# Performance work log

Measured on AMD Instinct MI355X. Metric: run time of the kernel, lower is better.

The kernel has to match this reference:

```python
import jax, jax.numpy as jnp
import numpy as np

B, L, D_IN = 32, 1024, 256
EMB, OUT = 128, 128


def setup_inputs() -> dict:
    key = jax.random.key(0)
    ks = jax.random.split(key, 8)
    traj = jax.random.normal(ks[0], (B, L, D_IN), dtype=jnp.float32)
    traj_length = jax.random.randint(ks[1], (B,), 0, L).astype(jnp.int64)
    s_in = 1.0 / np.sqrt(D_IN)
    W_ge = jax.random.uniform(ks[2], (D_IN, EMB), jnp.float32, -s_in, s_in)
    b_ge = jax.random.uniform(ks[3], (EMB,), jnp.float32, -s_in, s_in)
    W_eg = jax.random.uniform(ks[4], (D_IN, EMB), jnp.float32, -s_in, s_in)
    b_eg = jax.random.uniform(ks[5], (EMB,), jnp.float32, -s_in, s_in)
    Wg = jax.random.normal(ks[6], (EMB, OUT), dtype=jnp.float32)
    ln_gamma = jnp.ones((OUT,), jnp.float32)
    ln_beta = jnp.zeros((OUT,), jnp.float32)
    return {"traj": traj, "traj_length": traj_length, "W_ge": W_ge, "b_ge": b_ge,
            "W_eg": W_eg, "b_eg": b_eg, "Wg": Wg, "ln_gamma": ln_gamma, "ln_beta": ln_beta}


def layer_norm(x, gamma, beta, eps=1e-5):
    mu = jnp.mean(x, axis=-1, keepdims=True)
    var = jnp.var(x, axis=-1, keepdims=True)
    return (x - mu) * jax.lax.rsqrt(var + eps) * gamma + beta


def reference(traj, traj_length, W_ge, b_ge, W_eg, b_eg, Wg, ln_gamma, ln_beta):
    Bd, Ld, _ = traj.shape
    # node embeddings for similarity
    EA = traj @ W_ge + b_ge                                   # [B, L, EMB]
    sim = jax.nn.relu(jnp.einsum('bie,bje->bij', EA, EA))     # [B, L, L]
    mask = (jnp.arange(Ld)[None, :] < traj_length[:, None]).astype(jnp.float32)  # [B, L]
    # NOTE: original zeroes masked scores (not -inf); exp(0)=1 still contributes
    sim = sim * mask[:, None, :]
    A = jax.nn.softmax(sim, axis=-1)                          # [B, L, L]
    Eg = traj @ W_eg + b_eg                                   # [B, L, EMB]
    theta = Eg @ Wg                                           # [B, L, OUT]
    propagated = jnp.einsum('bij,bjd->bid', A, theta)         # [B, L, OUT]
    propagated = layer_norm(propagated, ln_gamma, ln_beta)
    return propagated * mask[:, :, None]
```

## Files before the change

kernel.cpp:

```cpp
#include <hip/hip_runtime.h>
#include <hip/hip_bf16.h>

#define B_   32
#define L_   1024
#define DIN  256

typedef __bf16 bf16x8 __attribute__((ext_vector_type(8)));
typedef float  f32x4  __attribute__((ext_vector_type(4)));
typedef unsigned short u16;

union U8 { u16 s[8]; bf16x8 v; };
union VU { uint2 p[2]; bf16x8 v; };

__device__ __forceinline__ u16 f2b(float f) {
  union { float f; unsigned u; } v; v.f = f;
  unsigned r = (v.u + 0x7FFFu + ((v.u >> 16) & 1u)) >> 16;
  return (u16)r;
}
__device__ __forceinline__ float b2f(u16 h) {
  union { unsigned u; float f; } c; c.u = ((unsigned)h) << 16;
  return c.f;
}

#define TR16_0(dst, addr) \
  asm volatile("ds_read_b64_tr_b16 %0, %1 offset:0" : "=&v"(dst) : "v"(addr))
#define TR16_128(dst, addr) \
  asm volatile("ds_read_b64_tr_b16 %0, %1 offset:128" : "=&v"(dst) : "v"(addr))

__global__ __launch_bounds__(256) void k_fold(
    const float* __restrict__ W_ge, const float* __restrict__ b_eg,
    const float* __restrict__ W_eg, const float* __restrict__ Wg,
    u16* __restrict__ WbT, float* __restrict__ bc, float* __restrict__ TT) {
  int idx = blockIdx.x * 256 + threadIdx.x;
  if (idx < 32768) {
    int d = idx >> 7, o = idx & 127;
    float s = 0.f;
    for (int k = 0; k < 128; ++k) s += W_eg[d * 128 + k] * Wg[k * 128 + o];
    WbT[(128 + o) * 256 + d] = f2b(s);
  } else if (idx < 65536) {
    int i = idx - 32768; int d = i >> 7, o = i & 127;
    WbT[o * 256 + d] = f2b(W_ge[d * 128 + o]);
  } else if (idx < 65664) {
    int o = idx - 65536;
    float s = 0.f;
    for (int k = 0; k < 128; ++k) s += b_eg[k] * Wg[k * 128 + o];
    bc[o] = s;
  } else if (idx < 65664 + 4096) {
    TT[idx - 65664] = 0.f;
  }
}

__global__ __launch_bounds__(512) void k_embed(
    const float* __restrict__ traj, const u16* __restrict__ WbT,
    const float* __restrict__ b_ge, const float* __restrict__ bc,
    const int* __restrict__ lens,
    u16* __restrict__ EA, u16* __restrict__ TH, float* __restrict__ TT) {
  __shared__ u16 Ws[256][264];
  __shared__ float tailLds[128];
  const int tid = threadIdx.x;
  const int wv = tid >> 6, ln = tid & 63;
  const int li = ln & 15, g = ln >> 4;
  const int b   = blockIdx.x >> 3;
  const int rl0 = (blockIdx.x & 7) * 128;
  const int len = lens[b];
  const int rw  = rl0 + wv * 16 + li;
  const size_t row = (size_t)b * L_ + rw;
  const int nd0 = (rl0 >= len) ? 8 : 0;
  const bool doTail = (rl0 + 128 > len);

  if (tid < 128) tailLds[tid] = 0.f;

  {
    const u16* src = &WbT[(tid >> 1) * 256 + (tid & 1) * 128];
    u16* dst = &Ws[tid >> 1][(tid & 1) * 128];
#pragma unroll
    for (int i = 0; i < 16; ++i)
      *(bf16x8*)&dst[i * 8] = *(const bf16x8*)&src[i * 8];
  }

  bf16x8 tf[8];
  {
    const float* tp = &traj[row * DIN];
#pragma unroll
    for (int t = 0; t < 8; ++t) {
      float4 v0 = *(const float4*)(tp + t * 32 + g * 8);
      float4 v1 = *(const float4*)(tp + t * 32 + g * 8 + 4);
      U8 bu;
      bu.s[0]=f2b(v0.x); bu.s[1]=f2b(v0.y); bu.s[2]=f2b(v0.z); bu.s[3]=f2b(v0.w);
      bu.s[4]=f2b(v1.x); bu.s[5]=f2b(v1.y); bu.s[6]=f2b(v1.z); bu.s[7]=f2b(v1.w);
      tf[t] = bu.v;
    }
  }
  __syncthreads();

  f32x4 acc[16] = {};
#pragma unroll
  for (int kc = 0; kc < 8; ++kc) {
#pragma unroll
    for (int nd = 0; nd < 16; ++nd) {
      if (nd >= nd0) {
        bf16x8 afrag = *(const bf16x8*)&Ws[nd * 16 + li][kc * 32 + g * 8];
        acc[nd] = __builtin_amdgcn_mfma_f32_16x16x32_bf16(afrag, tf[kc], acc[nd], 0, 0, 0);
      }
    }
  }

#pragma unroll
  for (int nd = 0; nd < 16; ++nd) {
    if (nd < nd0) continue;
    int ncol = nd * 16 + 4 * g;
    float fv[4];
    u16 pk[4];
#pragma unroll
    for (int r = 0; r < 4; ++r) {
      int n = ncol + r;
      float bias = (n < 128) ? b_ge[n] : bc[n - 128];
      fv[r] = acc[nd][r] + bias;
      pk[r] = f2b(fv[r]);
    }
    u16* dst = (ncol < 128) ? &EA[row * 128 + ncol]
                            : &TH[row * 128 + (ncol - 128)];
    *(uint2*)dst = *(uint2*)pk;

    if (nd >= 8 && doTail) {
      float tv[4];
#pragma unroll
      for (int r = 0; r < 4; ++r) tv[r] = (rw >= len) ? fv[r] : 0.f;
#pragma unroll
      for (int d = 1; d < 16; d <<= 1)
#pragma unroll
        for (int r = 0; r < 4; ++r) tv[r] += __shfl_xor(tv[r], d, 16);
      if (li == 0) {
#pragma unroll
        for (int r = 0; r < 4; ++r)
          atomicAdd(&tailLds[(nd - 8) * 16 + 4 * g + r], tv[r]);
      }
    }
  }
  __syncthreads();
  if (tid < 128) {
    float v = tailLds[tid];
    if (v != 0.f) atomicAdd(&TT[b * 128 + tid], v);
  }
}

#define PSTR 40

__global__ __launch_bounds__(256) void k_attn(
    const u16* __restrict__ EA, const u16* __restrict__ TH,
    const float* __restrict__ TT, const int* __restrict__ lens,
    const float* __restrict__ gamma, const float* __restrict__ beta,
    float* __restrict__ out) {
  const int b  = blockIdx.y;
  const int i0 = blockIdx.x * 32;
  const int len = lens[b];
  const int tid = threadIdx.x;
  const size_t obase = ((size_t)b * L_ + i0) * 128;

  if (i0 >= len) {
    float4 z = {0.f, 0.f, 0.f, 0.f};
    for (int q = tid; q < 1024; q += 256) *(float4*)&out[obase + (size_t)q * 4] = z;
    return;
  }

  __shared__ u16 Kl[2][2][4096];
  __shared__ u16 Vl[2][2][4096];
  __shared__ u16 Pl[4][640];
  __shared__ float MLm[32], MLl[32];
  __shared__ u16 MGb[32][136];

  const int wv = tid >> 6;
  const int h = wv & 1, p = wv >> 1;
  const int ln = tid & 63, li = ln & 15, g = ln >> 4;
  const int ptid = tid & 127;
  const int jr = ptid >> 2, ch = ptid & 3;
  const size_t ebase = (size_t)b * L_ * 128;

  u16* pl = Pl[wv];

  bf16x8 qf[4];
  {
    const u16* qp = &EA[ebase + (size_t)(i0 + h * 16 + li) * 128 + g * 8];
#pragma unroll
    for (int kc = 0; kc < 4; ++kc) qf[kc] = *(const bf16x8*)&qp[kc * 32];
  }

  f32x4 Oa[8] = {};
  float m[4] = {0.f, 0.f, 0.f, 0.f};
  float lsum[4] = {0.f, 0.f, 0.f, 0.f};

  const int njt = (len + 31) >> 5;
  const int kiter = (njt + 1) >> 1;

  bf16x8 kreg[4], vreg[4];
  {
    const int t0 = (p < njt) ? p : (njt - 1);
    const u16* ks = &EA[ebase + (size_t)(t0 * 32 + jr) * 128];
    const u16* vs = &TH[ebase + (size_t)(t0 * 32 + jr) * 128];
#pragma unroll
    for (int k = 0; k < 4; ++k) {
      kreg[k] = *(const bf16x8*)(ks + (ch + 4 * k) * 8);
      vreg[k] = *(const bf16x8*)(vs + (ch + 4 * k) * 8);
    }
  }

  for (int kk = 0; kk < kiter; ++kk) {
    const int t = 2 * kk + p;
    u16* kd = Kl[p][kk & 1];
    u16* vd = Vl[p][kk & 1];
#pragma unroll
    for (int k = 0; k < 4; ++k) {
      int cq = ch + 4 * k;
      int cb = cq * 16;
      *(bf16x8*)((char*)kd + jr * 256 + (cb ^ ((jr & 7) << 4))) = kreg[k];
      *(bf16x8*)&vd[(cq >> 1) * 512 + jr * 16 + (cq & 1) * 8] = vreg[k];
    }
    if (kk + 1 < kiter) {
      int tn = 2 * (kk + 1) + p; if (tn > njt - 1) tn = njt - 1;
      const u16* ks = &EA[ebase + (size_t)(tn * 32 + jr) * 128];
      const u16* vs = &TH[ebase + (size_t)(tn * 32 + jr) * 128];
#pragma unroll
      for (int k = 0; k < 4; ++k) {
        kreg[k] = *(const bf16x8*)(ks + (ch + 4 * k) * 8);
        vreg[k] = *(const bf16x8*)(vs + (ch + 4 * k) * 8);
      }
    }
    __syncthreads();
    if (t < njt) {
      const int j0 = t * 32;
      f32x4 S[2] = {};
#pragma unroll
      for (int n = 0; n < 2; ++n) {
        int krow = n * 16 + li;
        const char* kb = (const char*)kd + krow * 256;
#pragma unroll
        for (int kc = 0; kc < 4; ++kc) {
          bf16x8 kf = *(const bf16x8*)(kb + ((kc * 64 + g * 16) ^ ((krow & 7) << 4)));
          S[n] = __builtin_amdgcn_mfma_f32_16x16x32_bf16(qf[kc], kf, S[n], 0, 0, 0);
        }
      }
      const unsigned vtr = (unsigned)(size_t)vd + g * 256 + li * 8;
      uint2 vr[16];
#pragma unroll
      for (int t8 = 0; t8 < 8; ++t8) {
        unsigned a = vtr + t8 * 1024;
        TR16_0(vr[2 * t8], a);
        TR16_128(vr[2 * t8 + 1], a);
      }
      const bool v0 = (j0 + li) < len;
      const bool v1 = (j0 + 16 + li) < len;
      float x[4];
#pragma unroll
      for (int r = 0; r < 4; ++r) {
        float s0 = v0 ? fmaxf(S[0][r], 0.f) : 0.f;
        float s1 = v1 ? fmaxf(S[1][r], 0.f) : 0.f;
        S[0][r] = s0; S[1][r] = s1;
        x[r] = fmaxf(s0, s1);
      }
#pragma unroll
      for (int d = 1; d < 16; d <<= 1)
#pragma unroll
        for (int r = 0; r < 4; ++r) x[r] = fmaxf(x[r], __shfl_xor(x[r], d, 16));

      float p0[4], p1[4], fac[4], y[4];
#pragma unroll
      for (int r = 0; r < 4; ++r) {
        float mt = fmaxf(m[r], x[r]);
        fac[r] = __expf(m[r] - mt);
        m[r] = mt;
        p0[r] = v0 ? __expf(S[0][r] - mt) : 0.f;
        p1[r] = v1 ? __expf(S[1][r] - mt) : 0.f;
        y[r] = p0[r] + p1[r];
      }
#pragma unroll
      for (int d = 1; d < 16; d <<= 1)
#pragma unroll
        for (int r = 0; r < 4; ++r) y[r] += __shfl_xor(y[r], d, 16);
#pragma unroll
      for (int r = 0; r < 4; ++r) lsum[r] = lsum[r] * fac[r] + y[r];
#pragma unroll
      for (int t8 = 0; t8 < 8; ++t8)
#pragma unroll
        for (int r = 0; r < 4; ++r) Oa[t8][r] *= fac[r];

#pragma unroll
      for (int r = 0; r < 4; ++r) {
        pl[(4 * g + r) * PSTR + li]      = f2b(p0[r]);
        pl[(4 * g + r) * PSTR + 16 + li] = f2b(p1[r]);
      }
      bf16x8 pf = *(const bf16x8*)&pl[li * PSTR + g * 8];

      asm volatile("s_waitcnt lgkmcnt(0)" ::: "memory");
      __builtin_amdgcn_sched_barrier(0);

#pragma unroll
      for (int t8 = 0; t8 < 8; ++t8) {
        VU vu; vu.p[0] = vr[2 * t8]; vu.p[1] = vr[2 * t8 + 1];
        Oa[t8] = __builtin_amdgcn_mfma_f32_16x16x32_bf16(pf, vu.v, Oa[t8], 0, 0, 0);
      }
    }
  }

  __syncthreads();
  if (p == 1) {
#pragma unroll
    for (int r = 0; r < 4; ++r) {
      int rr = h * 16 + 4 * g + r;
      if (li == 0) { MLm[rr] = m[r]; MLl[rr] = lsum[r]; }
#pragma unroll
      for (int t8 = 0; t8 < 8; ++t8)
        MGb[rr][t8 * 16 + li] = f2b(Oa[t8][r]);
    }
  }
  __syncthreads();
  if (p != 0) return;

#pragma unroll
  for (int r = 0; r < 4; ++r) {
    int rr = h * 16 + 4 * g + r;
    float m1 = MLm[rr], l1 = MLl[rr];
    float ms = fmaxf(m[r], m1);
    float f0 = __expf(m[r] - ms), f1 = __expf(m1 - ms);
    lsum[r] = lsum[r] * f0 + l1 * f1;
    m[r] = ms;
#pragma unroll
    for (int t8 = 0; t8 < 8; ++t8)
      Oa[t8][r] = Oa[t8][r] * f0 + b2f(MGb[rr][t8 * 16 + li]) * f1;
  }

  {
    float tt8[8];
#pragma unroll
    for (int t8 = 0; t8 < 8; ++t8) tt8[t8] = TT[b * 128 + t8 * 16 + li];
#pragma unroll
    for (int r = 0; r < 4; ++r) {
      float wt = __expf(-m[r]);
      lsum[r] += wt * (float)(L_ - len);
#pragma unroll
      for (int t8 = 0; t8 < 8; ++t8) Oa[t8][r] += wt * tt8[t8];
    }
  }

  float sm[4] = {0.f, 0.f, 0.f, 0.f}, sq[4] = {0.f, 0.f, 0.f, 0.f};
#pragma unroll
  for (int r = 0; r < 4; ++r) {
    float inv = 1.f / lsum[r];
#pragma unroll
    for (int t8 = 0; t8 < 8; ++t8) {
      float val = Oa[t8][r] * inv;
      Oa[t8][r] = val;
      sm[r] += val; sq[r] += val * val;
    }
  }
#pragma unroll
  for (int d = 1; d < 16; d <<= 1)
#pragma unroll
    for (int r = 0; r < 4; ++r) {
      sm[r] += __shfl_xor(sm[r], d, 16);
      sq[r] += __shfl_xor(sq[r], d, 16);
    }

  const int irow = i0 + h * 16;
#pragma unroll
  for (int r = 0; r < 4; ++r) {
    float mu   = sm[r] * (1.f / 128.f);
    float var  = sq[r] * (1.f / 128.f) - mu * mu;
    float rstd = rsqrtf(var + 1e-5f);
    int i = irow + 4 * g + r;
    bool valid = i < len;
#pragma unroll
    for (int t8 = 0; t8 < 8; ++t8) {
      int dcol = t8 * 16 + li;
      float o = valid ? ((Oa[t8][r] - mu) * rstd * gamma[dcol] + beta[dcol]) : 0.f;
      out[((size_t)b * L_ + i) * 128 + dcol] = o;
    }
  }
}

extern "C" void kernel_launch(void* const* d_in, const int* in_sizes, int n_in,
                              void* d_out, int out_size, void* d_ws, size_t ws_size,
                              hipStream_t stream) {
  const float* traj  = (const float*)d_in[0];
  const int*   lens  = (const int*)d_in[1];
  const float* W_ge  = (const float*)d_in[2];
  const float* b_ge  = (const float*)d_in[3];
  const float* W_eg  = (const float*)d_in[4];
  const float* b_eg  = (const float*)d_in[5];
  const float* Wg    = (const float*)d_in[6];
  const float* gamma = (const float*)d_in[7];
  const float* beta  = (const float*)d_in[8];
  float* out = (float*)d_out;

  char* ws = (char*)d_ws;
  u16*   WbT = (u16*)ws;
  float* bc  = (float*)(ws + 131072);
  float* TT  = (float*)(ws + 131072 + 512);
  u16*   EA  = (u16*)(ws + 131072 + 512 + 16384);
  u16*   TH  = EA + (size_t)B_ * L_ * 128;

  k_fold<<<273, 256, 0, stream>>>(W_ge, b_eg, W_eg, Wg, WbT, bc, TT);
  k_embed<<<256, 512, 0, stream>>>(traj, WbT, b_ge, bc, lens, EA, TH, TT);
  k_attn<<<dim3(32, 32), 256, 0, stream>>>(EA, TH, TT, lens, gamma, beta, out);
}
```

Baseline: 173.7 us.

## Stage Wg in LDS for weight folding and stream embed weights from global

k_fold now has each block copy Wg into a 64 KB shared buffer. Each thread then computes one folded W_eg·Wg entry from LDS instead of re-reading Wg from global memory, and the blocks are remapped so each one covers two input rows. k_embed drops the 132 KB LDS copy of the packed weights and its per-block setup. It uses 64-row blocks of 256 threads, doubling the block count, and reads MFMA weight fragments straight from global memory through the cache. traj is now loaded and converted to bf16 inside the k loop rather than all up front. This trades LDS staging and occupancy limits for more global/L2 traffic on weight reads.

```diff
diff --git a/kernel.cpp b/kernel.cpp
--- a/kernel.cpp
+++ b/kernel.cpp
@@ -31,76 +31,71 @@
     const float* __restrict__ W_ge, const float* __restrict__ b_eg,
     const float* __restrict__ W_eg, const float* __restrict__ Wg,
     u16* __restrict__ WbT, float* __restrict__ bc, float* __restrict__ TT) {
-  int idx = blockIdx.x * 256 + threadIdx.x;
-  if (idx < 32768) {
-    int d = idx >> 7, o = idx & 127;
+  __shared__ float WgL[128 * 128];
+  const int blk = blockIdx.x, tid = threadIdx.x;
+  if (blk < 128) {
+    const float4* src = (const float4*)Wg;
+    float4* dst = (float4*)WgL;
+#pragma unroll
+    for (int i = 0; i < 16; ++i) dst[tid + i * 256] = src[tid + i * 256];
+    __syncthreads();
+    const int d = blk * 2 + (tid >> 7);
+    const int o = tid & 127;
+    const float* we = &W_eg[d * 128];
     float s = 0.f;
-    for (int k = 0; k < 128; ++k) s += W_eg[d * 128 + k] * Wg[k * 128 + o];
+#pragma unroll 8
+    for (int k = 0; k < 128; ++k) s += we[k] * WgL[k * 128 + o];
     WbT[(128 + o) * 256 + d] = f2b(s);
-  } else if (idx < 65536) {
-    int i = idx - 32768; int d = i >> 7, o = i & 127;
+  } else if (blk < 256) {
+    int i = (blk - 128) * 256 + tid;
+    int d = i >> 7, o = i & 127;
     WbT[o * 256 + d] = f2b(W_ge[d * 128 + o]);
-  } else if (idx < 65664) {
-    int o = idx - 65536;
-    float s = 0.f;
-    for (int k = 0; k < 128; ++k) s += b_eg[k] * Wg[k * 128 + o];
-    bc[o] = s;
-  } else if (idx < 65664 + 4096) {
-    TT[idx - 65664] = 0.f;
-  }
-}
-
-__global__ __launch_bounds__(512) void k_embed(
+  } else {
+    int i = (blk - 256) * 256 + tid;
+    if (i < 128) {
+      float s = 0.f;
+      for (int k = 0; k < 128; ++k) s += b_eg[k] * Wg[k * 128 + i];
+      bc[i] = s;
+    } else if (i < 128 + 4096) {
+      TT[i - 128] = 0.f;
+    }
+  }
+}
+
+__global__ __launch_bounds__(256) void k_embed(
     const float* __restrict__ traj, const u16* __restrict__ WbT,
     const float* __restrict__ b_ge, const float* __restrict__ bc,
     const int* __restrict__ lens,
     u16* __restrict__ EA, u16* __restrict__ TH, float* __restrict__ TT) {
-  __shared__ u16 Ws[256][264];
   __shared__ float tailLds[128];
   const int tid = threadIdx.x;
   const int wv = tid >> 6, ln = tid & 63;
   const int li = ln & 15, g = ln >> 4;
-  const int b   = blockIdx.x >> 3;
-  const int rl0 = (blockIdx.x & 7) * 128;
+  const int b   = blockIdx.x >> 4;
+  const int rl0 = (blockIdx.x & 15) * 64;
   const int len = lens[b];
   const int rw  = rl0 + wv * 16 + li;
   const size_t row = (size_t)b * L_ + rw;
   const int nd0 = (rl0 >= len) ? 8 : 0;
-  const bool doTail = (rl0 + 128 > len);
+  const bool doTail = (rl0 + 64 > len);
 
   if (tid < 128) tailLds[tid] = 0.f;
-
-  {
-    const u16* src = &WbT[(tid >> 1) * 256 + (tid & 1) * 128];
-    u16* dst = &Ws[tid >> 1][(tid & 1) * 128];
-#pragma unroll
-    for (int i = 0; i < 16; ++i)
-      *(bf16x8*)&dst[i * 8] = *(const bf16x8*)&src[i * 8];
-  }
-
-  bf16x8 tf[8];
-  {
-    const float* tp = &traj[row * DIN];
-#pragma unroll
-    for (int t = 0; t < 8; ++t) {
-      float4 v0 = *(const float4*)(tp + t * 32 + g * 8);
-      float4 v1 = *(const float4*)(tp + t * 32 + g * 8 + 4);
-      U8 bu;
-      bu.s[0]=f2b(v0.x); bu.s[1]=f2b(v0.y); bu.s[2]=f2b(v0.z); bu.s[3]=f2b(v0.w);
-      bu.s[4]=f2b(v1.x); bu.s[5]=f2b(v1.y); bu.s[6]=f2b(v1.z); bu.s[7]=f2b(v1.w);
-      tf[t] = bu.v;
-    }
-  }
   __syncthreads();
 
   f32x4 acc[16] = {};
-#pragma unroll
+  const float* tp = &traj[row * DIN];
+
   for (int kc = 0; kc < 8; ++kc) {
+    float4 v0 = *(const float4*)(tp + kc * 32 + g * 8);
+    float4 v1 = *(const float4*)(tp + kc * 32 + g * 8 + 4);
+    U8 bu;
+    bu.s[0]=f2b(v0.x); bu.s[1]=f2b(v0.y); bu.s[2]=f2b(v0.z); bu.s[3]=f2b(v0.w);
+    bu.s[4]=f2b(v1.x); bu.s[5]=f2b(v1.y); bu.s[6]=f2b(v1.z); bu.s[7]=f2b(v1.w);
 #pragma unroll
     for (int nd = 0; nd < 16; ++nd) {
       if (nd >= nd0) {
-        bf16x8 afrag = *(const bf16x8*)&Ws[nd * 16 + li][kc * 32 + g * 8];
-        acc[nd] = __builtin_amdgcn_mfma_f32_16x16x32_bf16(afrag, tf[kc], acc[nd], 0, 0, 0);
+        bf16x8 afrag = *(const bf16x8*)&WbT[(nd * 16 + li) * 256 + kc * 32 + g * 8];
+        acc[nd] = __builtin_amdgcn_mfma_f32_16x16x32_bf16(afrag, bu.v, acc[nd], 0, 0, 0);
       }
     }
   }
@@ -399,6 +394,6 @@
   u16*   TH  = EA + (size_t)B_ * L_ * 128;
 
   k_fold<<<273, 256, 0, stream>>>(W_ge, b_eg, W_eg, Wg, WbT, bc, TT);
-  k_embed<<<256, 512, 0, stream>>>(traj, WbT, b_ge, bc, lens, EA, TH, TT);
+  k_embed<<<512, 256, 0, stream>>>(traj, WbT, b_ge, bc, lens, EA, TH, TT);
   k_attn<<<dim3(32, 32), 256, 0, stream>>>(EA, TH, TT, lens, gamma, beta, out);
 }
```

After: 191.2 us. +10.1%, slower.
